# Kernel optimization log

Measured on AMD Instinct MI355X. Metric: run time of the kernel, lower is better.

The kernel has to match this reference:

```python
import jax, jax.numpy as jnp
import numpy as np

N_NODES = 20000
N_EDGES = 160000
D_IN = 512
D_HID = 512
D_OUT = 512
N_GRAPHS = 128


def setup_inputs() -> dict:
    key = jax.random.key(0)
    ks = jax.random.split(key, 10)
    x = jax.random.normal(ks[0], (N_NODES, D_IN), dtype=jnp.float32)
    edge_index = jax.random.randint(ks[1], (2, N_EDGES), 0, N_NODES, dtype=jnp.int64)
    batch = jnp.sort(jax.random.randint(ks[2], (N_NODES,), 0, N_GRAPHS, dtype=jnp.int64))
    s = 1.0 / np.sqrt(D_IN)
    W1 = jax.random.normal(ks[3], (D_IN, D_HID), dtype=jnp.float32) * s
    b1 = jnp.zeros((D_HID,), dtype=jnp.float32)
    W2 = jax.random.normal(ks[4], (D_HID, D_OUT), dtype=jnp.float32) * s
    b2 = jnp.zeros((D_OUT,), dtype=jnp.float32)
    Wlin = jax.random.normal(ks[5], (D_OUT, D_OUT), dtype=jnp.float32) * s
    blin = jnp.zeros((D_OUT,), dtype=jnp.float32)
    return {"x": x, "edge_index": edge_index, "batch": batch,
            "W1": W1, "b1": b1, "W2": W2, "b2": b2, "Wlin": Wlin, "blin": blin}


def _gcn_conv(h, src, dst, W, b, n_nodes):
    # PyG GCNConv: h' = D^{-1/2} (A + I) D^{-1/2} (h @ W) + b, self-loops added.
    h = h @ W
    deg = jax.ops.segment_sum(jnp.ones_like(dst, dtype=h.dtype), dst, num_segments=n_nodes)
    dis = jnp.where(deg > 0, jax.lax.rsqrt(jnp.maximum(deg, 1.0)), 0.0)
    norm = dis[src] * dis[dst]                      # [E+N]
    msg = h[src] * norm[:, None]                    # gather-scale
    out = jax.ops.segment_sum(msg, dst, num_segments=n_nodes)  # scatter-add
    return out + b


def reference(x, edge_index, batch, W1, b1, W2, b2, Wlin, blin):
    n = x.shape[0]
    # StandardScaler: per-feature zero-mean, unit (population) std
    mu = jnp.mean(x, axis=0)
    sd = jnp.std(x, axis=0)
    xs = (x - mu) / jnp.where(sd > 0, sd, 1.0)
    # add self-loops once, shared by both convs
    ar = jnp.arange(n, dtype=edge_index.dtype)
    src = jnp.concatenate([edge_index[0], ar])
    dst = jnp.concatenate([edge_index[1], ar])
    x1 = jax.nn.relu(_gcn_conv(xs, src, dst, W1, b1, n))
    # dropout is identity in eval mode
    x2 = _gcn_conv(x1, src, dst, W2, b2, n)
    # global_mean_pool over graph ids
    sums = jax.ops.segment_sum(x2, batch, num_segments=N_GRAPHS)
    cnts = jax.ops.segment_sum(jnp.ones((n,), dtype=x2.dtype), batch, num_segments=N_GRAPHS)
    pooled = sums / jnp.maximum(cnts, 1.0)[:, None]
    # (second dropout also identity in eval); module returns x3 (pre log_softmax)
    return pooled @ Wlin + blin
```

## Files before the change

### kernel.cpp

```cpp
#include <hip/hip_runtime.h>
#include <hip/hip_bf16.h>


#define NN 20000
#define NE 160000
#define DD 512
#define NG 128
#define PSLICE 16

typedef __attribute__((ext_vector_type(8))) short bf16x8;
typedef __attribute__((ext_vector_type(4))) float f32x4;

static __device__ __forceinline__ short f2bf(float f) {
    union { float f; unsigned u; } a; a.f = f;
    unsigned r = a.u + 0x7FFF + ((a.u >> 16) & 1);
    return (short)(r >> 16);
}
static __device__ __forceinline__ float bf2f(short s) {
    union { unsigned u; float f; } a; a.u = ((unsigned)(unsigned short)s) << 16;
    return a.f;
}

__global__ __launch_bounds__(256) void colstats_kernel(const float* __restrict__ x,
                                                       float* __restrict__ colsum,
                                                       float* __restrict__ colsq) {
    int c = blockIdx.x * 256 + threadIdx.x;
    int r0 = blockIdx.y * 100;
    float s = 0.f, sq = 0.f;
    for (int r = r0; r < r0 + 100; ++r) {
        float v = x[(size_t)r * DD + c];
        s += v;
        sq = fmaf(v, v, sq);
    }
    atomicAdd(&colsum[c], s);
    atomicAdd(&colsq[c], sq);
}

__global__ void finalize_kernel(const float* __restrict__ colsum, const float* __restrict__ colsq,
                                float* __restrict__ rstd, float* __restrict__ murs) {
    int c = threadIdx.x;
    float m = colsum[c] * (1.0f / NN);
    float var = colsq[c] * (1.0f / NN) - m * m;
    float sd = sqrtf(fmaxf(var, 0.0f));
    float rs = (sd > 0.0f) ? (1.0f / sd) : 1.0f;
    rstd[c] = rs;
    murs[c] = m * rs;
}

__global__ __launch_bounds__(256) void xsplit_kernel(const float* __restrict__ x,
                                                     const float* __restrict__ rstd,
                                                     const float* __restrict__ murs,
                                                     short* __restrict__ xh,
                                                     short* __restrict__ xl) {
    int idx = blockIdx.x * 256 + threadIdx.x;
    int c4 = (idx & 127) * 4;
    float4 v = *(const float4*)(x + (size_t)idx * 4);
    float4 rs = *(const float4*)(rstd + c4);
    float4 ms = *(const float4*)(murs + c4);
    float s0 = fmaf(v.x, rs.x, -ms.x), s1 = fmaf(v.y, rs.y, -ms.y);
    float s2 = fmaf(v.z, rs.z, -ms.z), s3 = fmaf(v.w, rs.w, -ms.w);
    short h0 = f2bf(s0), h1 = f2bf(s1), h2 = f2bf(s2), h3 = f2bf(s3);
    *(short4*)(xh + (size_t)idx * 4) = make_short4(h0, h1, h2, h3);
    *(short4*)(xl + (size_t)idx * 4) =
        make_short4(f2bf(s0 - bf2f(h0)), f2bf(s1 - bf2f(h1)),
                    f2bf(s2 - bf2f(h2)), f2bf(s3 - bf2f(h3)));
}

__global__ __launch_bounds__(256) void wsplit_kernel(const float* __restrict__ W1,
                                                     short* __restrict__ Wh,
                                                     short* __restrict__ Wl) {
    __shared__ float t[32][33];
    int bk = blockIdx.x * 32, bn = blockIdx.y * 32;
    int r = threadIdx.x >> 5, c = threadIdx.x & 31;
#pragma unroll
    for (int i = 0; i < 4; ++i) {
        int rr = r + i * 8;
        t[rr][c] = W1[(size_t)(bk + rr) * DD + bn + c];
    }
    __syncthreads();
#pragma unroll
    for (int i = 0; i < 4; ++i) {
        int rr = r + i * 8;
        float v = t[c][rr];
        short h = f2bf(v);
        short l = f2bf(v - bf2f(h));
        Wh[(size_t)(bn + rr) * DD + bk + c] = h;
        Wl[(size_t)(bn + rr) * DD + bk + c] = l;
    }
}

__global__ void deginit_kernel(int* __restrict__ deg) {
    int i = blockIdx.x * 256 + threadIdx.x;
    if (i < NN) deg[i] = 1;
}

__global__ void degcount_kernel(const int* __restrict__ dst, int* __restrict__ deg, int es) {
    int e = blockIdx.x * 256 + threadIdx.x;
    if (e < NE) {
        int d = dst[(size_t)e * es];
        if ((unsigned)d < (unsigned)NN) atomicAdd(&deg[d], 1);
    }
}

__global__ void dis_kernel(const int* __restrict__ deg, float* __restrict__ dis) {
    int i = blockIdx.x * 256 + threadIdx.x;
    if (i < NN) dis[i] = rsqrtf((float)deg[i]);
}

__global__ __launch_bounds__(1024) void scan_kernel(const int* __restrict__ deg,
                                                    int* __restrict__ rowptr,
                                                    int* __restrict__ cursor) {
    const int PER = 20;
    __shared__ int sums[1024];
    int t = threadIdx.x;
    int base = t * PER;
    int local[PER];
    int s = 0;
#pragma unroll
    for (int j = 0; j < PER; ++j) {
        int idx = base + j;
        int v = (idx < NN) ? (deg[idx] - 1) : 0;
        local[j] = s;
        s += v;
    }
    sums[t] = s;
    __syncthreads();
    for (int off = 1; off < 1024; off <<= 1) {
        int v = (t >= off) ? sums[t - off] : 0;
        __syncthreads();
        sums[t] += v;
        __syncthreads();
    }
    int prefix = (t == 0) ? 0 : sums[t - 1];
#pragma unroll
    for (int j = 0; j < PER; ++j) {
        int idx = base + j;
        if (idx <= NN) {
            int val = prefix + local[j];
            rowptr[idx] = val;
            if (idx < NN) cursor[idx] = val;
        }
    }
}

__global__ void scatter_kernel(const int* __restrict__ src, const int* __restrict__ dst,
                               int* __restrict__ cursor, int* __restrict__ csrsrc, int es) {
    int e = blockIdx.x * 256 + threadIdx.x;
    if (e < NE) {
        int d = dst[(size_t)e * es];
        int sN = src[(size_t)e * es];
        if ((unsigned)d < (unsigned)NN && (unsigned)sN < (unsigned)NN) {
            int slot = atomicAdd(&cursor[d], 1);
            csrsrc[slot] = sN;
        }
    }
}

__global__ __launch_bounds__(256) void gemm_mfma_kernel(const short* __restrict__ Ah_g,
                                                        const short* __restrict__ Al_g,
                                                        const short* __restrict__ Bh_g,
                                                        const short* __restrict__ Bl_g,
                                                        float* __restrict__ C,
                                                        int M) {
    __shared__ __attribute__((aligned(16))) short sAh[128][40];
    __shared__ __attribute__((aligned(16))) short sAl[128][40];
    __shared__ __attribute__((aligned(16))) short sBh[128][40];
    __shared__ __attribute__((aligned(16))) short sBl[128][40];
    int tid = threadIdx.x;
    int wave = tid >> 6, lane = tid & 63;
    int wm = (wave >> 1) * 64, wn = (wave & 1) * 64;
    int rowBase = blockIdx.x * 128, colBase = blockIdx.y * 128;
    int fr = lane & 15, kq = (lane >> 4) * 8;

    int s0 = tid, s1 = tid + 256;
    int r0 = s0 >> 2, k80 = (s0 & 3) * 8;
    int r1 = s1 >> 2, k81 = (s1 & 3) * 8;
    int ga0 = rowBase + r0, ga1 = rowBase + r1;
    int gb0 = colBase + r0, gb1 = colBase + r1;
    const bool av0 = ga0 < M, av1 = ga1 < M;

    f32x4 acc[4][4];
#pragma unroll
    for (int i = 0; i < 4; ++i)
#pragma unroll
        for (int j = 0; j < 4; ++j) acc[i][j] = (f32x4){0.f, 0.f, 0.f, 0.f};

    const bf16x8 z8 = {0, 0, 0, 0, 0, 0, 0, 0};
    bf16x8 rAh0, rAh1, rAl0, rAl1, rBh0, rBh1, rBl0, rBl1;

#define GLOAD(KK)                                                                      \
    do {                                                                               \
        rAh0 = av0 ? *(const bf16x8*)(Ah_g + (size_t)ga0 * DD + (KK) + k80) : z8;      \
        rAl0 = av0 ? *(const bf16x8*)(Al_g + (size_t)ga0 * DD + (KK) + k80) : z8;      \
        rAh1 = av1 ? *(const bf16x8*)(Ah_g + (size_t)ga1 * DD + (KK) + k81) : z8;      \
        rAl1 = av1 ? *(const bf16x8*)(Al_g + (size_t)ga1 * DD + (KK) + k81) : z8;      \
        rBh0 = *(const bf16x8*)(Bh_g + (size_t)gb0 * DD + (KK) + k80);                 \
        rBl0 = *(const bf16x8*)(Bl_g + (size_t)gb0 * DD + (KK) + k80);                 \
        rBh1 = *(const bf16x8*)(Bh_g + (size_t)gb1 * DD + (KK) + k81);                 \
        rBl1 = *(const bf16x8*)(Bl_g + (size_t)gb1 * DD + (KK) + k81);                 \
    } while (0)

    GLOAD(0);
    for (int step = 0; step < 16; ++step) {
        *(bf16x8*)&sAh[r0][k80] = rAh0;  *(bf16x8*)&sAl[r0][k80] = rAl0;
        *(bf16x8*)&sAh[r1][k81] = rAh1;  *(bf16x8*)&sAl[r1][k81] = rAl1;
        *(bf16x8*)&sBh[r0][k80] = rBh0;  *(bf16x8*)&sBl[r0][k80] = rBl0;
        *(bf16x8*)&sBh[r1][k81] = rBh1;  *(bf16x8*)&sBl[r1][k81] = rBl1;
        __syncthreads();
        if (step < 15) GLOAD((step + 1) * 32);

        bf16x8 fah[4], fal[4], fbh[4], fbl[4];
#pragma unroll
        for (int mi = 0; mi < 4; ++mi) {
            fah[mi] = *(const bf16x8*)&sAh[wm + mi * 16 + fr][kq];
            fal[mi] = *(const bf16x8*)&sAl[wm + mi * 16 + fr][kq];
        }
#pragma unroll
        for (int ni = 0; ni < 4; ++ni) {
            fbh[ni] = *(const bf16x8*)&sBh[wn + ni * 16 + fr][kq];
            fbl[ni] = *(const bf16x8*)&sBl[wn + ni * 16 + fr][kq];
        }
#pragma unroll
        for (int mi = 0; mi < 4; ++mi)
#pragma unroll
            for (int ni = 0; ni < 4; ++ni) {
                acc[mi][ni] = __builtin_amdgcn_mfma_f32_16x16x32_bf16(fah[mi], fbh[ni], acc[mi][ni], 0, 0, 0);
                acc[mi][ni] = __builtin_amdgcn_mfma_f32_16x16x32_bf16(fah[mi], fbl[ni], acc[mi][ni], 0, 0, 0);
                acc[mi][ni] = __builtin_amdgcn_mfma_f32_16x16x32_bf16(fal[mi], fbh[ni], acc[mi][ni], 0, 0, 0);
            }
        __syncthreads();
    }
#undef GLOAD

#pragma unroll
    for (int mi = 0; mi < 4; ++mi)
#pragma unroll
        for (int ni = 0; ni < 4; ++ni) {
            int col = colBase + wn + ni * 16 + fr;
            int row0 = rowBase + wm + mi * 16 + (lane >> 4) * 4;
#pragma unroll
            for (int r = 0; r < 4; ++r) {
                int row = row0 + r;
                if (row < M) C[(size_t)row * DD + col] = acc[mi][ni][r];
            }
        }
}

__global__ __launch_bounds__(256) void agg_kernel(const float* __restrict__ h,
                                                  float* __restrict__ out,
                                                  const float* __restrict__ dis,
                                                  const int* __restrict__ rowptr,
                                                  const int* __restrict__ csrsrc,
                                                  const float* __restrict__ bias,
                                                  int relu) {
    int i = blockIdx.x;
    int f = threadIdx.x * 2;
    float di = dis[i];
    float2 v = *(const float2*)(h + (size_t)i * DD + f);
    float accx = di * v.x, accy = di * v.y;
    int e0 = rowptr[i], e1 = rowptr[i + 1];
    if (e0 < e1) {
        int s = csrsrc[e0];
        float ds = dis[s];
        for (int e = e0; e < e1; ++e) {
            int   sn = 0;
            float dn = 0.f;
            if (e + 1 < e1) { sn = csrsrc[e + 1]; dn = dis[sn]; }
            float2 hv = *(const float2*)(h + (size_t)s * DD + f);
            accx = fmaf(ds, hv.x, accx);
            accy = fmaf(ds, hv.y, accy);
            s = sn; ds = dn;
        }
    }
    accx = fmaf(di, accx, bias[f]);
    accy = fmaf(di, accy, bias[f + 1]);
    if (relu) { accx = fmaxf(accx, 0.f); accy = fmaxf(accy, 0.f); }
    *(float2*)(out + (size_t)i * DD + f) = make_float2(accx, accy);
}

__global__ __launch_bounds__(256) void poolagg_kernel(const float* __restrict__ g1,
                                                      const int* __restrict__ batch, int bs,
                                                      const float* __restrict__ dis,
                                                      const int* __restrict__ rowptr,
                                                      const int* __restrict__ csrsrc,
                                                      float* __restrict__ part) {
    int g = blockIdx.x;
    int c = blockIdx.y * 256 + threadIdx.x;
    int sl = blockIdx.z;
    __shared__ int slo, shi;
    if (threadIdx.x == 0) {
        int lo = 0, hi = NN;
        while (lo < hi) { int m = (lo + hi) >> 1; if (batch[(size_t)m * bs] < g) lo = m + 1; else hi = m; }
        slo = lo;
        lo = slo; hi = NN;
        while (lo < hi) { int m = (lo + hi) >> 1; if (batch[(size_t)m * bs] < g + 1) lo = m + 1; else hi = m; }
        shi = lo;
    }
    __syncthreads();
    int lo = slo, hi = shi;
    int n = hi - lo;
    int a0 = lo + (int)(((long long)n * sl) / PSLICE);
    int a1 = lo + (int)(((long long)n * (sl + 1)) / PSLICE);
    float acc = 0.f;
    for (int i = a0; i < a1; ++i) {
        float di = dis[i];
        float t = 0.f;
        int e0 = rowptr[i], e1 = rowptr[i + 1];
        for (int e = e0; e < e1; ++e) {
            int s = csrsrc[e];
            t = fmaf(dis[s], g1[(size_t)s * DD + c], t);
        }
        float self = g1[(size_t)i * DD + c];
        acc = fmaf(di, fmaf(di, self, t), acc);
    }
    float inv = 1.0f / fmaxf((float)n, 1.0f);
    part[((size_t)sl * NG + g) * DD + c] = acc * inv;
}

__global__ __launch_bounds__(256) void final_kernel(const float* __restrict__ src, int nslice,
                                                    const float* __restrict__ W,
                                                    const float* __restrict__ bias,
                                                    float* __restrict__ dst) {
    __shared__ float p[DD];
    int g = blockIdx.x;
    int t = threadIdx.x;
    float s0 = 0.f, s1 = 0.f;
    for (int sl = 0; sl < nslice; ++sl) {
        s0 += src[((size_t)sl * NG + g) * DD + t];
        s1 += src[((size_t)sl * NG + g) * DD + t + 256];
    }
    p[t] = s0;
    p[t + 256] = s1;
    __syncthreads();
    float a0 = bias[t], a1 = bias[t + 256];
    for (int k = 0; k < DD; ++k) {
        float pk = p[k];
        a0 = fmaf(pk, W[(size_t)k * DD + t], a0);
        a1 = fmaf(pk, W[(size_t)k * DD + t + 256], a1);
    }
    dst[(size_t)g * DD + t] = a0;
    dst[(size_t)g * DD + t + 256] = a1;
}

extern "C" void kernel_launch(void* const* d_in, const int* in_sizes, int n_in,
                              void* d_out, int out_size, void* d_ws, size_t ws_size,
                              hipStream_t stream) {
    const float* x    = (const float*)d_in[0];
    const int*   ei   = (const int*)d_in[1];
    const int*   batch= (const int*)d_in[2];
    const float* W1   = (const float*)d_in[3];
    const float* b1   = (const float*)d_in[4];
    const float* W2   = (const float*)d_in[5];
    const float* b2   = (const float*)d_in[6];
    const float* Wlin = (const float*)d_in[7];
    const float* blin = (const float*)d_in[8];
    float* out = (float*)d_out;

    const int es = (in_sizes[1] == 2 * 2 * NE) ? 2 : 1;
    const int bs = (in_sizes[2] == 2 * NN) ? 2 : 1;
    const int* esrc = ei;
    const int* edst = ei + (size_t)NE * es;

    char* w = (char*)d_ws;
    auto alloc = [&](size_t bytes) { void* p = (void*)w; w += (bytes + 255) & ~(size_t)255; return p; };
    float* h      = (float*)alloc((size_t)NN * DD * 4);
    float* part   = h;
    float* g      = (float*)alloc((size_t)NN * DD * 4);
    short* xh     = (short*)g;
    short* xl     = (short*)g + (size_t)NN * DD;
    short* W1h    = (short*)alloc((size_t)DD * DD * 2);
    short* W1l    = (short*)alloc((size_t)DD * DD * 2);
    float* tbuf   = (float*)alloc((size_t)NG * DD * 4);
    float* rstd   = (float*)alloc(DD * 4);
    float* murs   = (float*)alloc(DD * 4);
    float* stats  = (float*)alloc(2 * DD * 4);
    float* dis    = (float*)alloc(NN * 4);
    int*   deg    = (int*)alloc(NN * 4);
    int*   rowptr = (int*)alloc((NN + 4) * 4);
    int*   cursor = (int*)alloc(NN * 4);
    int*   csrsrc = (int*)alloc(NE * 4);
    float* colsum = stats;
    float* colsq  = stats + DD;

    hipMemsetAsync(stats, 0, 2 * DD * 4, stream);
    colstats_kernel<<<dim3(2, 200), 256, 0, stream>>>(x, colsum, colsq);
    finalize_kernel<<<1, 512, 0, stream>>>(colsum, colsq, rstd, murs);
    xsplit_kernel<<<10000, 256, 0, stream>>>(x, rstd, murs, xh, xl);
    wsplit_kernel<<<dim3(16, 16), 256, 0, stream>>>(W1, W1h, W1l);

    deginit_kernel<<<(NN + 255) / 256, 256, 0, stream>>>(deg);
    degcount_kernel<<<NE / 256, 256, 0, stream>>>(edst, deg, es);
    dis_kernel<<<(NN + 255) / 256, 256, 0, stream>>>(deg, dis);
    scan_kernel<<<1, 1024, 0, stream>>>(deg, rowptr, cursor);
    scatter_kernel<<<NE / 256, 256, 0, stream>>>(esrc, edst, cursor, csrsrc, es);

    gemm_mfma_kernel<<<dim3((NN + 127) / 128, DD / 128), 256, 0, stream>>>(xh, xl, W1h, W1l, h, NN);
    agg_kernel<<<NN, 256, 0, stream>>>(h, g, dis, rowptr, csrsrc, b1, 1);
    poolagg_kernel<<<dim3(NG, 2, PSLICE), 256, 0, stream>>>(g, batch, bs, dis, rowptr, csrsrc, part);
    final_kernel<<<NG, 256, 0, stream>>>(part, PSLICE, W2, b2, tbuf);
    final_kernel<<<NG, 256, 0, stream>>>(tbuf, 1, Wlin, blin, out);
}
```

Measured before the change: 417.8 us.

## Replace pooled aggregation gather with a dense pooling-matrix GEMM

Builds a dense per-graph coefficient matrix C[graph][node] with atomics. C folds the second GCN aggregation and the mean pool into one linear operator, so pooled = C·g1. That product runs as a split-K fp32 tiled GEMM over 125 node chunks, and the final kernel sums the chunks and applies per-graph 1/n scaling. The aim is to replace the poorly coalesced per-edge gathers of poolagg with a regular dense GEMM. The cost is a 10 MB memset, atomic construction of C, and about 32 MB of partial results to write and reduce.

```diff
diff --git a/kernel.cpp b/kernel.cpp
--- a/kernel.cpp
+++ b/kernel.cpp
@@ -6,7 +6,8 @@
 #define NE 160000
 #define DD 512
 #define NG 128
-#define PSLICE 16
+#define PKC 160
+#define PNC 125
 
 typedef __attribute__((ext_vector_type(8))) short bf16x8;
 typedef __attribute__((ext_vector_type(4))) float f32x4;
@@ -154,6 +155,43 @@
             csrsrc[slot] = sN;
         }
     }
+}
+
+__global__ void cnode_kernel(const int* __restrict__ batch, int bs,
+                             const float* __restrict__ dis, float* __restrict__ Cf) {
+    int j = blockIdx.x * 256 + threadIdx.x;
+    if (j < NN) {
+        int G = batch[(size_t)j * bs];
+        if ((unsigned)G < (unsigned)NG) {
+            float d = dis[j];
+            atomicAdd(&Cf[(size_t)G * NN + j], d * d);
+        }
+    }
+}
+
+__global__ void cedge_kernel(const int* __restrict__ src, const int* __restrict__ dst, int es,
+                             const int* __restrict__ batch, int bs,
+                             const float* __restrict__ dis, float* __restrict__ Cf) {
+    int e = blockIdx.x * 256 + threadIdx.x;
+    if (e < NE) {
+        int i = dst[(size_t)e * es];
+        int s = src[(size_t)e * es];
+        if ((unsigned)i < (unsigned)NN && (unsigned)s < (unsigned)NN) {
+            int G = batch[(size_t)i * bs];
+            if ((unsigned)G < (unsigned)NG)
+                atomicAdd(&Cf[(size_t)G * NN + s], dis[i] * dis[s]);
+        }
+    }
+}
+
+__global__ void invn_kernel(const int* __restrict__ batch, int bs, float* __restrict__ inv_n) {
+    int g = threadIdx.x;
+    int lo = 0, hi = NN;
+    while (lo < hi) { int m = (lo + hi) >> 1; if (batch[(size_t)m * bs] < g) lo = m + 1; else hi = m; }
+    int l0 = lo;
+    lo = l0; hi = NN;
+    while (lo < hi) { int m = (lo + hi) >> 1; if (batch[(size_t)m * bs] < g + 1) lo = m + 1; else hi = m; }
+    inv_n[g] = 1.0f / fmaxf((float)(lo - l0), 1.0f);
 }
 
 __global__ __launch_bounds__(256) void gemm_mfma_kernel(const short* __restrict__ Ah_g,
@@ -278,49 +316,74 @@
     *(float2*)(out + (size_t)i * DD + f) = make_float2(accx, accy);
 }
 
-__global__ __launch_bounds__(256) void poolagg_kernel(const float* __restrict__ g1,
-                                                      const int* __restrict__ batch, int bs,
-                                                      const float* __restrict__ dis,
-                                                      const int* __restrict__ rowptr,
-                                                      const int* __restrict__ csrsrc,
-                                                      float* __restrict__ part) {
-    int g = blockIdx.x;
-    int c = blockIdx.y * 256 + threadIdx.x;
-    int sl = blockIdx.z;
-    __shared__ int slo, shi;
-    if (threadIdx.x == 0) {
-        int lo = 0, hi = NN;
-        while (lo < hi) { int m = (lo + hi) >> 1; if (batch[(size_t)m * bs] < g) lo = m + 1; else hi = m; }
-        slo = lo;
-        lo = slo; hi = NN;
-        while (lo < hi) { int m = (lo + hi) >> 1; if (batch[(size_t)m * bs] < g + 1) lo = m + 1; else hi = m; }
-        shi = lo;
-    }
-    __syncthreads();
-    int lo = slo, hi = shi;
-    int n = hi - lo;
-    int a0 = lo + (int)(((long long)n * sl) / PSLICE);
-    int a1 = lo + (int)(((long long)n * (sl + 1)) / PSLICE);
-    float acc = 0.f;
-    for (int i = a0; i < a1; ++i) {
-        float di = dis[i];
-        float t = 0.f;
-        int e0 = rowptr[i], e1 = rowptr[i + 1];
-        for (int e = e0; e < e1; ++e) {
-            int s = csrsrc[e];
-            t = fmaf(dis[s], g1[(size_t)s * DD + c], t);
-        }
-        float self = g1[(size_t)i * DD + c];
-        acc = fmaf(di, fmaf(di, self, t), acc);
-    }
-    float inv = 1.0f / fmaxf((float)n, 1.0f);
-    part[((size_t)sl * NG + g) * DD + c] = acc * inv;
+__global__ __launch_bounds__(256) void pgemm_kernel(const float* __restrict__ A,
+                                                    const float* __restrict__ B,
+                                                    float* __restrict__ part) {
+    __shared__ float As[16][132];
+    __shared__ float Bs[16][128];
+    int tid = threadIdx.x;
+    int tx = tid & 15, ty = tid >> 4;
+    int colBase = blockIdx.x * 128;
+    int kc = blockIdx.y;
+    int kBase = kc * PKC;
+
+    float acc[8][8];
+#pragma unroll
+    for (int i = 0; i < 8; ++i)
+#pragma unroll
+        for (int j = 0; j < 8; ++j) acc[i][j] = 0.f;
+
+    for (int k0 = kBase; k0 < kBase + PKC; k0 += 16) {
+#pragma unroll
+        for (int i = 0; i < 2; ++i) {
+            int lin = tid + i * 256;
+            int r = lin >> 2, c4 = (lin & 3) * 4;
+            float4 v = *(const float4*)(A + (size_t)r * NN + k0 + c4);
+            As[c4 + 0][r] = v.x;
+            As[c4 + 1][r] = v.y;
+            As[c4 + 2][r] = v.z;
+            As[c4 + 3][r] = v.w;
+        }
+#pragma unroll
+        for (int i = 0; i < 2; ++i) {
+            int lin = tid + i * 256;
+            int kk = lin >> 5, c4 = (lin & 31) * 4;
+            *(float4*)&Bs[kk][c4] = *(const float4*)(B + (size_t)(k0 + kk) * DD + colBase + c4);
+        }
+        __syncthreads();
+#pragma unroll
+        for (int kk = 0; kk < 16; ++kk) {
+            float a[8], b[8];
+            *(float4*)&a[0] = *(const float4*)&As[kk][ty * 4];
+            *(float4*)&a[4] = *(const float4*)&As[kk][64 + ty * 4];
+            *(float4*)&b[0] = *(const float4*)&Bs[kk][tx * 4];
+            *(float4*)&b[4] = *(const float4*)&Bs[kk][64 + tx * 4];
+#pragma unroll
+            for (int i = 0; i < 8; ++i)
+#pragma unroll
+                for (int j = 0; j < 8; ++j) acc[i][j] = fmaf(a[i], b[j], acc[i][j]);
+        }
+        __syncthreads();
+    }
+
+    float* dst = part + (size_t)kc * NG * DD;
+#pragma unroll
+    for (int i = 0; i < 8; ++i) {
+        int r = (i < 4) ? (ty * 4 + i) : (64 + ty * 4 + (i - 4));
+        int c0 = colBase + tx * 4;
+        int c1c = colBase + 64 + tx * 4;
+        *(float4*)(dst + (size_t)r * DD + c0) =
+            make_float4(acc[i][0], acc[i][1], acc[i][2], acc[i][3]);
+        *(float4*)(dst + (size_t)r * DD + c1c) =
+            make_float4(acc[i][4], acc[i][5], acc[i][6], acc[i][7]);
+    }
 }
 
 __global__ __launch_bounds__(256) void final_kernel(const float* __restrict__ src, int nslice,
                                                     const float* __restrict__ W,
                                                     const float* __restrict__ bias,
-                                                    float* __restrict__ dst) {
+                                                    float* __restrict__ dst,
+                                                    const float* __restrict__ scale) {
     __shared__ float p[DD];
     int g = blockIdx.x;
     int t = threadIdx.x;
@@ -329,8 +392,9 @@
         s0 += src[((size_t)sl * NG + g) * DD + t];
         s1 += src[((size_t)sl * NG + g) * DD + t + 256];
     }
-    p[t] = s0;
-    p[t + 256] = s1;
+    float sc = scale ? scale[g] : 1.0f;
+    p[t] = s0 * sc;
+    p[t + 256] = s1 * sc;
     __syncthreads();
     float a0 = bias[t], a1 = bias[t + 256];
     for (int k = 0; k < DD; ++k) {
@@ -370,7 +434,9 @@
     short* xl     = (short*)g + (size_t)NN * DD;
     short* W1h    = (short*)alloc((size_t)DD * DD * 2);
     short* W1l    = (short*)alloc((size_t)DD * DD * 2);
+    float* Cf     = (float*)alloc((size_t)NG * NN * 4);
     float* tbuf   = (float*)alloc((size_t)NG * DD * 4);
+    float* inv_n  = (float*)alloc(NG * 4);
     float* rstd   = (float*)alloc(DD * 4);
     float* murs   = (float*)alloc(DD * 4);
     float* stats  = (float*)alloc(2 * DD * 4);
@@ -394,9 +460,14 @@
     scan_kernel<<<1, 1024, 0, stream>>>(deg, rowptr, cursor);
     scatter_kernel<<<NE / 256, 256, 0, stream>>>(esrc, edst, cursor, csrsrc, es);
 
+    hipMemsetAsync(Cf, 0, (size_t)NG * NN * 4, stream);
+    cnode_kernel<<<(NN + 255) / 256, 256, 0, stream>>>(batch, bs, dis, Cf);
+    cedge_kernel<<<NE / 256, 256, 0, stream>>>(esrc, edst, es, batch, bs, dis, Cf);
+    invn_kernel<<<1, NG, 0, stream>>>(batch, bs, inv_n);
+
     gemm_mfma_kernel<<<dim3((NN + 127) / 128, DD / 128), 256, 0, stream>>>(xh, xl, W1h, W1l, h, NN);
     agg_kernel<<<NN, 256, 0, stream>>>(h, g, dis, rowptr, csrsrc, b1, 1);
-    poolagg_kernel<<<dim3(NG, 2, PSLICE), 256, 0, stream>>>(g, batch, bs, dis, rowptr, csrsrc, part);
-    final_kernel<<<NG, 256, 0, stream>>>(part, PSLICE, W2, b2, tbuf);
-    final_kernel<<<NG, 256, 0, stream>>>(tbuf, 1, Wlin, blin, out);
-}
+    pgemm_kernel<<<dim3(4, PNC), 256, 0, stream>>>(Cf, g, part);
+    final_kernel<<<NG, 256, 0, stream>>>(part, PNC, W2, b2, tbuf, inv_n);
+    final_kernel<<<NG, 256, 0, stream>>>(tbuf, 1, Wlin, blin, out, nullptr);
+}
```

Measured after the change: 418.2 us. About the same (+0.1%).
